# Optimization experiments

Measured on AMD Instinct MI355X. Metric: run time of the kernel, lower is better.

## Reference

```python
import jax, jax.numpy as jnp
import numpy as np

N = 100000      # nodes
E = 1200000     # edges
D = 64          # feature dim
RW = 3          # round_window
L = 2           # num_layers
EPS = -1.0      # GIN init_eps -> (1+eps)*h + neighbor_sum == pure neighbor sum
LN_EPS = 1e-5   # torch LayerNorm default eps


def _ln(x):
    # LayerNorm over feature dim, elementwise_affine=False
    mu = jnp.mean(x, axis=-1, keepdims=True)
    var = jnp.var(x, axis=-1, keepdims=True)
    return (x - mu) * jax.lax.rsqrt(var + LN_EPS)


def _gin(h, src, dst):
    # DGL GINConv(None, 'sum'): (1+eps)*h_dst + sum_{src->dst} h_src
    agg = jax.ops.segment_sum(h[src], dst, num_segments=N)
    return (1.0 + EPS) * h + agg


def setup_inputs() -> dict:
    key = jax.random.key(0)
    k1, k2, k3, k4 = jax.random.split(key, 4)
    feature = jax.random.normal(k1, (N, D), dtype=jnp.float32)
    age = jax.random.randint(k2, (N,), 0, RW)
    src = jax.random.randint(k3, (E,), 0, N)
    dst = jax.random.randint(k4, (E,), 0, N)
    return {"feature": feature, "age": age, "src": src, "dst": dst}


def reference(feature, age, src, dst):
    hn = _ln(feature)  # normalize the (tiled) input features
    # window w keeps nodes with age >= w
    mask = (jnp.arange(RW)[:, None] <= age[None, :]).astype(hn.dtype)  # [RW, N]
    h0 = hn[None, :, :] * mask[:, :, None]  # [RW, N, D]
    windows = []
    for w in range(RW):  # small fixed round_window
        h = h0[w]
        feats = [h]
        for _ in range(L):
            h = jax.nn.relu(_ln(_gin(h, src, dst)))
            feats.append(h)
        windows.append(jnp.concatenate(feats, axis=1))  # [N, (L+1)*D]
    h_self = windows[0]
    # temporal_agg == 'mean_final'
    h_temp = jnp.mean(jnp.stack([windows[0] - windows[i] for i in range(1, RW)]), axis=0)
    return jnp.concatenate([h_self, h_temp], axis=1)  # [N, 2*(L+1)*D]
```

## Files before the change

kernel.cpp:

```cpp
#include <hip/hip_runtime.h>
#include <hip/hip_bf16.h>

constexpr int NN  = 100000;
constexpr int EE  = 1200000;
constexpr int D   = 64;
constexpr int CAP = 64;
constexpr float LN_EPS = 1e-5f;

__global__ void zero_int_kernel(int* __restrict__ p, int n) {
    int i = blockIdx.x * blockDim.x + threadIdx.x;
    if (i < n) p[i] = 0;
}

__global__ void fillpad_kernel(const int* __restrict__ src, const int* __restrict__ dst,
                               const int* __restrict__ age, int* __restrict__ cnt,
                               int* __restrict__ packed) {
    int e = blockIdx.x * blockDim.x + threadIdx.x;
    if (e >= EE) return;
    int d = dst[e];
    int slot = atomicAdd(&cnt[d], 1);
    if (slot < CAP) {
        int s = src[e];
        packed[(size_t)d * CAP + slot] = s | (age[s] << 17);
    }
}

__device__ __forceinline__ float2 bf22f2(ushort2 u) {
    float2 r;
    r.x = __uint_as_float((unsigned)u.x << 16);
    r.y = __uint_as_float((unsigned)u.y << 16);
    return r;
}

__device__ __forceinline__ ushort2 f2bf2(float2 v) {
    __hip_bfloat16 a = __float2bfloat16(v.x);
    __hip_bfloat16 b = __float2bfloat16(v.y);
    ushort2 u;
    u.x = *(const unsigned short*)&a;
    u.y = *(const unsigned short*)&b;
    return u;
}

__device__ __forceinline__ float2 ln_relu_pair(float2 a, bool relu) {
    float s = a.x + a.y;
    #pragma unroll
    for (int m = 1; m < 32; m <<= 1) s += __shfl_xor(s, m);
    float mu = s * (1.f / 64.f);
    float dx = a.x - mu, dy = a.y - mu;
    float q = dx * dx + dy * dy;
    #pragma unroll
    for (int m = 1; m < 32; m <<= 1) q += __shfl_xor(q, m);
    float rs = rsqrtf(q * (1.f / 64.f) + LN_EPS);
    float2 r;
    r.x = dx * rs;
    r.y = dy * rs;
    if (relu) { r.x = fmaxf(r.x, 0.f); r.y = fmaxf(r.y, 0.f); }
    return r;
}

__global__ void ln_kernel(const float* __restrict__ x, __hip_bfloat16* __restrict__ ybf,
                          int nrows) {
    int gid  = blockIdx.x * blockDim.x + threadIdx.x;
    int row  = gid >> 6;
    int lane = gid & 63;
    if (row >= nrows) return;
    size_t i = (size_t)row * D + lane;
    float v = x[i];
    float s = v;
    #pragma unroll
    for (int m = 1; m < 64; m <<= 1) s += __shfl_xor(s, m);
    float mu = s * (1.f / 64.f);
    float d = v - mu;
    float q = d * d;
    #pragma unroll
    for (int m = 1; m < 64; m <<= 1) q += __shfl_xor(q, m);
    float r = d * rsqrtf(q * (1.f / 64.f) + LN_EPS);
    __hip_bfloat16 b = __float2bfloat16(r);
    ybf[i] = b;
}

__global__ void gather1_kernel(const __hip_bfloat16* __restrict__ hnbf,
                               const int* __restrict__ cnt,
                               const int* __restrict__ packed,
                               __hip_bfloat16* __restrict__ A1bf,
                               float* __restrict__ out) {
    int gid  = blockIdx.x * blockDim.x + threadIdx.x;
    int node = gid >> 6;
    int lane = gid & 63;
    if (node >= NN) return;
    int sl = lane & 31;
    int h  = lane >> 5;
    int n  = min(cnt[node], CAP);
    const int* pl = packed + (size_t)node * CAP;
    float2 a0 = {0.f, 0.f}, a1 = {0.f, 0.f}, a2 = {0.f, 0.f};

    int C = n >> 2;
    for (int c = h; c < C; c += 2) {
        int4 pa = *reinterpret_cast<const int4*>(pl + 4 * c);
        int p[4] = {pa.x, pa.y, pa.z, pa.w};
        #pragma unroll
        for (int k = 0; k < 4; ++k) {
            const ushort2* row = reinterpret_cast<const ushort2*>(
                hnbf + (size_t)(p[k] & 0x1FFFF) * D);
            float2 v = bf22f2(row[sl]);
            int g = p[k] >> 17;
            a0.x += v.x; a0.y += v.y;
            if (g >= 1) { a1.x += v.x; a1.y += v.y; }
            if (g >= 2) { a2.x += v.x; a2.y += v.y; }
        }
    }
    if (h == 0) {
        for (int i = 4 * C; i < n; ++i) {
            int p = pl[i];
            const ushort2* row = reinterpret_cast<const ushort2*>(
                hnbf + (size_t)(p & 0x1FFFF) * D);
            float2 v = bf22f2(row[sl]);
            int g = p >> 17;
            a0.x += v.x; a0.y += v.y;
            if (g >= 1) { a1.x += v.x; a1.y += v.y; }
            if (g >= 2) { a2.x += v.x; a2.y += v.y; }
        }
    }
    a0.x += __shfl_xor(a0.x, 32); a0.y += __shfl_xor(a0.y, 32);
    a1.x += __shfl_xor(a1.x, 32); a1.y += __shfl_xor(a1.y, 32);
    a2.x += __shfl_xor(a2.x, 32); a2.y += __shfl_xor(a2.y, 32);

    float2 r0 = ln_relu_pair(a0, true);
    float2 r1 = ln_relu_pair(a1, true);
    float2 r2 = ln_relu_pair(a2, true);

    ushort2* rw = reinterpret_cast<ushort2*>(A1bf + (size_t)node * (3 * D));
    float* ob = out + (size_t)node * 384;
    if (h == 0) {
        rw[sl] = f2bf2(r0);
        reinterpret_cast<float2*>(ob + 64)[sl] = r0;
    } else {
        rw[32 + sl] = f2bf2(r1);
        rw[64 + sl] = f2bf2(r2);
        float2 o4;
        o4.x = r0.x - 0.5f * (r1.x + r2.x);
        o4.y = r0.y - 0.5f * (r1.y + r2.y);
        reinterpret_cast<float2*>(ob + 256)[sl] = o4;
    }
}

__global__ void gather2_kernel(const __hip_bfloat16* __restrict__ hnbf,
                               const __hip_bfloat16* __restrict__ A1bf,
                               const int* __restrict__ cnt, const int* __restrict__ packed,
                               const int* __restrict__ age, float* __restrict__ out) {
    int gid  = blockIdx.x * blockDim.x + threadIdx.x;
    int node = gid >> 6;
    int lane = gid & 63;
    if (node >= NN) return;
    int sl = lane & 31;
    int h  = lane >> 5;
    int n  = min(cnt[node], CAP);
    const int* pl = packed + (size_t)node * CAP;
    float2 a0 = {0.f, 0.f}, a1 = {0.f, 0.f}, a2 = {0.f, 0.f};

    int C = n >> 2;
    for (int c = h; c < C; c += 2) {
        int4 pa = *reinterpret_cast<const int4*>(pl + 4 * c);
        int p[4] = {pa.x, pa.y, pa.z, pa.w};
        #pragma unroll
        for (int k = 0; k < 4; ++k) {
            const ushort2* row = reinterpret_cast<const ushort2*>(
                A1bf + (size_t)(p[k] & 0x1FFFF) * (3 * D));
            float2 v0 = bf22f2(row[sl]);
            float2 v1 = bf22f2(row[32 + sl]);
            float2 v2 = bf22f2(row[64 + sl]);
            a0.x += v0.x; a0.y += v0.y;
            a1.x += v1.x; a1.y += v1.y;
            a2.x += v2.x; a2.y += v2.y;
        }
    }
    if (h == 0) {
        for (int i = 4 * C; i < n; ++i) {
            const ushort2* row = reinterpret_cast<const ushort2*>(
                A1bf + (size_t)(pl[i] & 0x1FFFF) * (3 * D));
            float2 v0 = bf22f2(row[sl]);
            float2 v1 = bf22f2(row[32 + sl]);
            float2 v2 = bf22f2(row[64 + sl]);
            a0.x += v0.x; a0.y += v0.y;
            a1.x += v1.x; a1.y += v1.y;
            a2.x += v2.x; a2.y += v2.y;
        }
    }
    a0.x += __shfl_xor(a0.x, 32); a0.y += __shfl_xor(a0.y, 32);
    a1.x += __shfl_xor(a1.x, 32); a1.y += __shfl_xor(a1.y, 32);
    a2.x += __shfl_xor(a2.x, 32); a2.y += __shfl_xor(a2.y, 32);

    float2 h20 = ln_relu_pair(a0, true);
    float2 h21 = ln_relu_pair(a1, true);
    float2 h22 = ln_relu_pair(a2, true);

    float2 hnv = bf22f2(reinterpret_cast<const ushort2*>(
        hnbf + (size_t)node * D)[sl]);
    int ag = age[node];
    float f = 1.f - 0.5f * (float)((ag >= 1) + (ag >= 2));
    float* ob = out + (size_t)node * 384;
    if (h == 0) {
        reinterpret_cast<float2*>(ob)[sl] = hnv;
        reinterpret_cast<float2*>(ob + 128)[sl] = h20;
    } else {
        float2 o3, o5;
        o3.x = hnv.x * f;
        o3.y = hnv.y * f;
        o5.x = h20.x - 0.5f * (h21.x + h22.x);
        o5.y = h20.y - 0.5f * (h21.y + h22.y);
        reinterpret_cast<float2*>(ob + 192)[sl] = o3;
        reinterpret_cast<float2*>(ob + 320)[sl] = o5;
    }
}

extern "C" void kernel_launch(void* const* d_in, const int* in_sizes, int n_in,
                              void* d_out, int out_size, void* d_ws, size_t ws_size,
                              hipStream_t stream) {
    const float* feature = (const float*)d_in[0];
    const int*   age     = (const int*)d_in[1];
    const int*   src     = (const int*)d_in[2];
    const int*   dst     = (const int*)d_in[3];
    float* out = (float*)d_out;

    size_t nd = (size_t)NN * D;
    __hip_bfloat16* hnbf = (__hip_bfloat16*)d_ws;
    __hip_bfloat16* A1bf = hnbf + nd;
    int* cnt    = (int*)(A1bf + 3 * nd);
    int* packed = cnt + NN;

    zero_int_kernel<<<(NN + 255) / 256, 256, 0, stream>>>(cnt, NN);
    fillpad_kernel<<<(EE + 255) / 256, 256, 0, stream>>>(src, dst, age, cnt, packed);
    ln_kernel<<<(int)((nd + 255) / 256), 256, 0, stream>>>(feature, hnbf, NN);
    gather1_kernel<<<(NN * 64 + 255) / 256, 256, 0, stream>>>(hnbf, cnt, packed, A1bf, out);
    gather2_kernel<<<(NN * 64 + 255) / 256, 256, 0, stream>>>(hnbf, A1bf, cnt, packed,
                                                              age, out);
}
```

Before: 234.7 us.

## Partition edge binning by XCD-local destination ranges and fold counter zeroing into LN

Replaces the one-thread-per-edge atomic fill with a grid where each block is mapped to one of 8 XCDs (by blockIdx & 7) and only handles edges whose destination falls in that XCD's node range. The aim is to keep each node's counter atomics and packed-slot writes inside a single XCD's L2, avoiding cross-die coherence traffic. In exchange, every XCD group reads the full dst array, so dst is read eight times. Zeroing the counters is also moved into the LayerNorm kernel, which removes one launch.

```diff
diff --git a/kernel.cpp b/kernel.cpp
--- a/kernel.cpp
+++ b/kernel.cpp
@@ -6,22 +6,31 @@
 constexpr int D   = 64;
 constexpr int CAP = 64;
 constexpr float LN_EPS = 1e-5f;
-
-__global__ void zero_int_kernel(int* __restrict__ p, int n) {
-    int i = blockIdx.x * blockDim.x + threadIdx.x;
-    if (i < n) p[i] = 0;
-}
-
-__global__ void fillpad_kernel(const int* __restrict__ src, const int* __restrict__ dst,
-                               const int* __restrict__ age, int* __restrict__ cnt,
-                               int* __restrict__ packed) {
-    int e = blockIdx.x * blockDim.x + threadIdx.x;
-    if (e >= EE) return;
-    int d = dst[e];
-    int slot = atomicAdd(&cnt[d], 1);
-    if (slot < CAP) {
-        int s = src[e];
-        packed[(size_t)d * CAP + slot] = s | (age[s] << 17);
+constexpr int NXCD = 8;
+constexpr int NPX  = (NN + NXCD - 1) / NXCD;
+constexpr int FILL_GRP = 256;
+constexpr int FILL_BLOCKS = NXCD * FILL_GRP;
+
+__global__ void fillx_kernel(const int* __restrict__ src, const int* __restrict__ dst,
+                             const int* __restrict__ age, int* __restrict__ cnt,
+                             int* __restrict__ packed) {
+    int bid = blockIdx.x;
+    int xcd = bid & 7;
+    int grp = bid >> 3;
+    int lo = xcd * NPX;
+    int hi = min(lo + NPX, NN);
+    int per = (EE + FILL_GRP - 1) / FILL_GRP;
+    int e0 = grp * per;
+    int e1 = min(e0 + per, EE);
+    for (int e = e0 + (int)threadIdx.x; e < e1; e += (int)blockDim.x) {
+        int d = dst[e];
+        if (d >= lo && d < hi) {
+            int slot = atomicAdd(&cnt[d], 1);
+            if (slot < CAP) {
+                int s = src[e];
+                packed[(size_t)d * CAP + slot] = s | (age[s] << 17);
+            }
+        }
     }
 }
 
@@ -59,8 +68,9 @@
 }
 
 __global__ void ln_kernel(const float* __restrict__ x, __hip_bfloat16* __restrict__ ybf,
-                          int nrows) {
+                          int* __restrict__ cnt, int nrows) {
     int gid  = blockIdx.x * blockDim.x + threadIdx.x;
+    if (gid < NN) cnt[gid] = 0;
     int row  = gid >> 6;
     int lane = gid & 63;
     if (row >= nrows) return;
@@ -75,8 +85,7 @@
     #pragma unroll
     for (int m = 1; m < 64; m <<= 1) q += __shfl_xor(q, m);
     float r = d * rsqrtf(q * (1.f / 64.f) + LN_EPS);
-    __hip_bfloat16 b = __float2bfloat16(r);
-    ybf[i] = b;
+    ybf[i] = __float2bfloat16(r);
 }
 
 __global__ void gather1_kernel(const __hip_bfloat16* __restrict__ hnbf,
@@ -228,9 +237,8 @@
     int* cnt    = (int*)(A1bf + 3 * nd);
     int* packed = cnt + NN;
 
-    zero_int_kernel<<<(NN + 255) / 256, 256, 0, stream>>>(cnt, NN);
-    fillpad_kernel<<<(EE + 255) / 256, 256, 0, stream>>>(src, dst, age, cnt, packed);
-    ln_kernel<<<(int)((nd + 255) / 256), 256, 0, stream>>>(feature, hnbf, NN);
+    ln_kernel<<<(int)((nd + 255) / 256), 256, 0, stream>>>(feature, hnbf, cnt, NN);
+    fillx_kernel<<<FILL_BLOCKS, 256, 0, stream>>>(src, dst, age, cnt, packed);
     gather1_kernel<<<(NN * 64 + 255) / 256, 256, 0, stream>>>(hnbf, cnt, packed, A1bf, out);
     gather2_kernel<<<(NN * 64 + 255) / 256, 256, 0, stream>>>(hnbf, A1bf, cnt, packed,
                                                               age, out);
```

New measurement: 218.5 us. -6.9%, faster.
